# Kernel optimization log

Measured on AMD Instinct MI355X. Metric: run time of the kernel, lower is better.

## Reference

```python
import jax, jax.numpy as jnp
import numpy as np

CAP_FACTOR = 1.25


def _moe_top1(x, wg, w1, b1, w2, b2):
    """Top-1 switch MoE with capacity-based token dropping.
    x: [T, d]; wg: [d, E]; w1: [E, d, f]; b1: [E, f]; w2: [E, f, d]; b2: [E, d].
    """
    T, d = x.shape
    E = wg.shape[1]
    cap = int(CAP_FACTOR * T / E)
    probs = jax.nn.softmax(x @ wg, axis=-1)            # [T, E]
    idx = jnp.argmax(probs, axis=-1)                   # [T] expert assignment
    gate = jnp.max(probs, axis=-1)                     # [T] gate prob
    oh = jax.nn.one_hot(idx, E, dtype=jnp.int32)       # [T, E]
    # position of each token within its expert's buffer
    pos = (jnp.cumsum(oh, axis=0) * oh).sum(-1) - 1    # [T]
    keep = pos < cap                                   # drop tokens over capacity
    pos_w = jnp.where(keep, pos, cap)                  # dropped -> overflow slot
    # dispatch: scatter tokens into per-expert buffers [E, cap+1, d]
    buf = jnp.zeros((E, cap + 1, d), dtype=x.dtype).at[idx, pos_w].set(x)
    buf = buf[:, :cap]                                 # slice off overflow slot
    # grouped expert FFN
    h = jax.nn.relu(jnp.einsum('ecd,edf->ecf', buf, w1) + b1[:, None, :])
    eo = jnp.einsum('ecf,efd->ecd', h, w2) + b2[:, None, :]
    # combine: gather each token's expert output, scale by gate prob, zero dropped
    pos_g = jnp.minimum(pos_w, cap - 1)
    out = eo[idx, pos_g] * (gate * keep.astype(x.dtype))[:, None]
    return out


def setup_inputs():
    key = jax.random.key(0)
    ks = jax.random.split(key, 12)
    B, S, d, dff, E1, E2 = 8, 2048, 1024, 4096, 8, 16
    s = lambda fan: np.float32(1.0 / np.sqrt(fan))
    return dict(
        x=jax.random.normal(ks[0], (B, S, d), jnp.float32),
        y=jax.random.randint(ks[1], (B,), 0, d),
        wg1=jax.random.normal(ks[2], (d, E1), jnp.float32) * s(d),
        w1a=jax.random.normal(ks[3], (E1, d, dff), jnp.float32) * s(d),
        b1a=jnp.zeros((E1, dff), jnp.float32),
        w2a=jax.random.normal(ks[4], (E1, dff, d), jnp.float32) * s(dff),
        b2a=jnp.zeros((E1, d), jnp.float32),
        wg2=jax.random.normal(ks[5], (d, E2), jnp.float32) * s(d),
        w1b=jax.random.normal(ks[6], (E2, d, dff), jnp.float32) * s(d),
        b1b=jnp.zeros((E2, dff), jnp.float32),
        w2b=jax.random.normal(ks[7], (E2, dff, d), jnp.float32) * s(dff),
        b2b=jnp.zeros((E2, d), jnp.float32),
    )


def reference(x, y, wg1, w1a, b1a, w2a, b2a, wg2, w1b, b1b, w2b, b2b):
    B, S, d = x.shape
    xf = x.reshape(B * S, d)
    m1 = _moe_top1(xf, wg1, w1a, b1a, w2a, b2a)        # moe1(x)
    m2 = _moe_top1(m1, wg2, w1b, b1b, w2b, b2b)        # moe2(moe_out)
    resid = x + m2.reshape(B, S, d)                    # residual add
    sent = resid.mean(axis=1)                          # [B, d] mean-pool -> logits
    logp = jax.nn.log_softmax(sent, axis=-1)
    return -logp[jnp.arange(B), y].mean()              # cross-entropy loss
```

## Files before the change

### kernel.cpp

```cpp
#include <hip/hip_runtime.h>
#include <hip/hip_bf16.h>
#include <cstdint>
#include <cstddef>

#define B_    8
#define S_    2048
#define D_    1024
#define DFF_  4096
#define E1_   8
#define E2_   16
#define T_    (B_*S_)
#define CAP1_ 2560
#define CAP2_ 1280
#define EC_   20480

typedef __bf16 bf16x8 __attribute__((ext_vector_type(8)));
typedef float  f32x4  __attribute__((ext_vector_type(4)));

__device__ __forceinline__ unsigned short f2bf(float x) {
  return __builtin_bit_cast(unsigned short, (__bf16)x);
}

template<int E>
__global__ __launch_bounds__(256)
void gate_kernel(const float* __restrict__ X, const float* __restrict__ WG,
                 int* __restrict__ idxO, float* __restrict__ gateO) {
  const int lane = threadIdx.x & 63;
  const int wv   = threadIdx.x >> 6;
  const int t    = blockIdx.x * 4 + wv;
  const float* xr = X + (size_t)t * D_;
  float acc[E];
#pragma unroll
  for (int e = 0; e < E; ++e) acc[e] = 0.f;
#pragma unroll
  for (int i = 0; i < 4; ++i) {
    float4 xv = *(const float4*)(xr + i * 256 + lane * 4);
    int kb = i * 256 + lane * 4;
#pragma unroll
    for (int j = 0; j < 4; ++j) {
      float xs = (&xv.x)[j];
      const float* wr = WG + (size_t)(kb + j) * E;
#pragma unroll
      for (int e = 0; e < E; ++e) acc[e] += xs * wr[e];
    }
  }
#pragma unroll
  for (int e = 0; e < E; ++e) {
    float v = acc[e];
#pragma unroll
    for (int s = 32; s >= 1; s >>= 1) v += __shfl_xor(v, s, 64);
    acc[e] = v;
  }
  if (lane == 0) {
    float mx = acc[0]; int mi = 0;
#pragma unroll
    for (int e = 1; e < E; ++e) if (acc[e] > mx) { mx = acc[e]; mi = e; }
    float s = 0.f;
#pragma unroll
    for (int e = 0; e < E; ++e) s += expf(acc[e] - mx);
    idxO[t]  = mi;
    gateO[t] = 1.0f / s;
  }
}

__global__ __launch_bounds__(1024)
void scan_kernel(const int* __restrict__ idx, int E, int cap,
                 int* __restrict__ pos, int* __restrict__ kept) {
  __shared__ int cnt[16][17];
  __shared__ int gbase[16];
  const int tid = threadIdx.x;
  const int w = tid >> 6, lane = tid & 63;
  if (tid < E) gbase[tid] = 0;
  __syncthreads();
  const unsigned long long lt = (lane == 63) ? 0xFFFFFFFFFFFFFFFFull >> 1
                                             : ((1ull << lane) - 1ull);
  for (int it = 0; it < T_ / 1024; ++it) {
    int t = it * 1024 + tid;
    int mi = idx[t];
    int rank = 0;
    for (int e = 0; e < E; ++e) {
      unsigned long long m = __ballot(mi == e);
      if (lane == 0) cnt[w][e] = __popcll(m);
      if (mi == e) rank = __popcll(m & lt);
    }
    __syncthreads();
    int off = 0;
    for (int w2 = 0; w2 < w; ++w2) off += cnt[w2][mi];
    pos[t] = gbase[mi] + off + rank;
    __syncthreads();
    if (tid < E) {
      int tot = 0;
      for (int w2 = 0; w2 < 16; ++w2) tot += cnt[w2][tid];
      gbase[tid] += tot;
    }
    __syncthreads();
  }
  if (tid < E) kept[tid] = min(gbase[tid], cap);
}

__global__ __launch_bounds__(64)
void scatter_kernel(const float* __restrict__ X, const int* __restrict__ idx,
                    const int* __restrict__ pos, int cap,
                    unsigned short* __restrict__ xbuf, int* __restrict__ tokmap,
                    float* __restrict__ mzero) {
  const int t = blockIdx.x;
  const int lane = threadIdx.x;
  const int p = pos[t];
  if (p < cap) {
    const size_t dst = ((size_t)idx[t] * cap + p) * D_;
    const float* xr = X + (size_t)t * D_;
#pragma unroll
    for (int i = 0; i < 4; ++i) {
      float4 v = *(const float4*)(xr + i * 256 + lane * 4);
      ushort4 o;
      o.x = f2bf(v.x); o.y = f2bf(v.y); o.z = f2bf(v.z); o.w = f2bf(v.w);
      *(ushort4*)(xbuf + dst + i * 256 + lane * 4) = o;
    }
    if (lane == 0) tokmap[(size_t)idx[t] * cap + p] = t;
  } else {
    float4 z = {0.f, 0.f, 0.f, 0.f};
    float* mr = mzero + (size_t)t * D_;
#pragma unroll
    for (int i = 0; i < 4; ++i) *(float4*)(mr + i * 256 + lane * 4) = z;
  }
}

__global__ __launch_bounds__(256)
void wtrans_kernel(const float* __restrict__ src, unsigned short* __restrict__ dst,
                   int K, int N) {
  __shared__ float t[64][65];
  const int tid = threadIdx.x;
  const size_t eo = (size_t)blockIdx.z * K * N;
  const int k0 = blockIdx.y * 64, n0 = blockIdx.x * 64;
  const float* s = src + eo + (size_t)k0 * N + n0;
  unsigned short* d = dst + eo + (size_t)n0 * K + k0;
#pragma unroll
  for (int i = 0; i < 4; ++i) {
    int k = i * 16 + (tid >> 4);
    int n4 = (tid & 15) * 4;
    float4 v = *(const float4*)(s + (size_t)k * N + n4);
    t[k][n4] = v.x; t[k][n4 + 1] = v.y; t[k][n4 + 2] = v.z; t[k][n4 + 3] = v.w;
  }
  __syncthreads();
#pragma unroll
  for (int i = 0; i < 4; ++i) {
    int n = i * 16 + (tid >> 4);
    int k4 = (tid & 15) * 4;
    ushort4 o;
    o.x = f2bf(t[k4][n]);     o.y = f2bf(t[k4 + 1][n]);
    o.z = f2bf(t[k4 + 2][n]); o.w = f2bf(t[k4 + 3][n]);
    *(ushort4*)(d + (size_t)n * K + k4) = o;
  }
}

#define STG(BASEPTR, H, KT, SLOT) do {                                          \
    const unsigned short* _s = (BASEPTR) + (size_t)((H) * 128) * K + (KT) + st_off; \
    __builtin_amdgcn_global_load_lds((const __attribute__((address_space(1))) void*)_s, \
        (__attribute__((address_space(3))) void*)(smem + (SLOT) + dst0), 16, 0, 0);   \
    __builtin_amdgcn_global_load_lds((const __attribute__((address_space(1))) void*)(_s + (size_t)64 * K), \
        (__attribute__((address_space(3))) void*)(smem + (SLOT) + 8192 + dst0), 16, 0, 0); \
  } while (0)

#define RDA(BUF, MH) do { _Pragma("unroll")                                     \
    for (int m_ = 0; m_ < 4; ++m_) {                                            \
      const char* _p = smem + (BUF) * 65536 + aslot + ((MH) * 4 + m_) * 2048;   \
      af[m_][0] = *(const bf16x8*)(_p + va);                                    \
      af[m_][1] = *(const bf16x8*)(_p + (va ^ 64)); } } while (0)

#define RDB(BUF, NH) do { _Pragma("unroll")                                     \
    for (int j_ = 0; j_ < 2; ++j_) {                                            \
      const char* _p = smem + (BUF) * 65536 + bslot + ((NH) * 2 + j_) * 2048;   \
      bf[(NH) * 2 + j_][0] = *(const bf16x8*)(_p + vb);                         \
      bf[(NH) * 2 + j_][1] = *(const bf16x8*)(_p + (vb ^ 64)); } } while (0)

#define QUAD(MH, NH) do {                                                       \
    __builtin_amdgcn_s_setprio(1);                                              \
    _Pragma("unroll") for (int m_ = 0; m_ < 4; ++m_)                            \
    _Pragma("unroll") for (int j_ = 0; j_ < 2; ++j_)                            \
    _Pragma("unroll") for (int k_ = 0; k_ < 2; ++k_)                            \
      acc[(MH) * 4 + m_][(NH) * 2 + j_] = __builtin_amdgcn_mfma_f32_16x16x32_bf16( \
          af[m_][k_], bf[(NH) * 2 + j_][k_], acc[(MH) * 4 + m_][(NH) * 2 + j_], 0, 0, 0); \
    __builtin_amdgcn_s_setprio(0);                                              \
  } while (0)

#define LGKM0 do { asm volatile("s_waitcnt lgkmcnt(0)" ::: "memory");           \
                   __builtin_amdgcn_sched_barrier(0); } while (0)
#define BAR   __builtin_amdgcn_s_barrier()
#define VM4   asm volatile("s_waitcnt vmcnt(4)" ::: "memory")
#define VM0   asm volatile("s_waitcnt vmcnt(0)" ::: "memory")

template<int MODE>
__global__ __launch_bounds__(512, 2)
void moe_gemm(const unsigned short* __restrict__ A,
              const unsigned short* __restrict__ BT,
              const float* __restrict__ bias, int K, int N, int cap, int nbcnt,
              const int* __restrict__ kept,
              unsigned short* __restrict__ Hout, float* __restrict__ Mout,
              const int* __restrict__ tokmap, const float* __restrict__ gate) {
  __shared__ char smem[131072];
  const int tid  = threadIdx.x;
  const int lane = tid & 63;
  const int wv   = tid >> 6;
  const int wr   = wv >> 2;
  const int wc   = wv & 3;

  const int nwg = gridDim.x;
  const int wg  = (blockIdx.x & 7) * (nwg >> 3) + (blockIdx.x >> 3);
  const int per_grp = nbcnt * 4;
  const int grp = wg / per_grp;
  const int rem = wg - grp * per_grp;
  const int mb  = grp * 4 + (rem & 3);
  const int nb  = rem >> 2;

  const int e  = (mb * 256) / cap;
  const int r0 = mb * 256 - e * cap;
  const int kept_e = kept[e];
  if (r0 >= kept_e) return;
  const unsigned short* Ab = A + (size_t)(mb * 256) * K;
  const unsigned short* Bb = BT + ((size_t)e * N + (size_t)nb * 256) * K;

  f32x4 acc[8][4];
#pragma unroll
  for (int m = 0; m < 8; ++m)
#pragma unroll
    for (int n = 0; n < 4; ++n) acc[m][n] = (f32x4){0.f, 0.f, 0.f, 0.f};

  const int scol   = ((tid & 7) ^ ((tid >> 3) & 7)) * 8;
  const size_t st_off = (size_t)(tid >> 3) * K + scol;
  const int dst0   = tid * 16;

  const int r16 = lane & 15;
  const int g16 = (lane >> 4) * 16;
  const int swz = (r16 & 7) * 16;
  const int va  = r16 * 128 + (g16 ^ swz);
  const int vb  = (wc & 1) * 8192 + va;
  const int aslot = wr * 16384;
  const int bslot = 32768 + (wc >> 1) * 16384;
  bf16x8 af[4][2], bf[4][2];

  STG(Ab, 0, 0, 0);
  STG(Ab, 1, 0, 16384);
  STG(Bb, 0, 0, 32768);
  STG(Bb, 1, 0, 49152);
  STG(Bb, 0, 64, 65536 + 32768);
  STG(Bb, 1, 64, 65536 + 49152);
  VM4; BAR;

  const int NI = K >> 7;
  for (int i = 0; i < NI; ++i) {
    const bool last = (i == NI - 1);
    const int kt1 = (2 * i + 1) << 6;
    const int kt2 = (2 * i + 2) << 6;
    const int kt3 = (2 * i + 3) << 6;

    RDA(0, 0); RDB(0, 0);
    STG(Ab, 0, kt1, 65536);
    BAR; LGKM0; QUAD(0, 0); BAR;
    RDB(0, 1);
    STG(Ab, 1, kt1, 65536 + 16384);
    BAR; LGKM0; QUAD(0, 1); BAR;
    RDA(0, 1);
    if (!last) STG(Bb, 0, kt2, 32768);
    BAR; LGKM0; QUAD(1, 1); BAR;
    if (!last) { STG(Bb, 1, kt2, 49152); VM4; } else { VM0; }
    BAR; __builtin_amdgcn_sched_barrier(0);
    QUAD(1, 0); BAR;
    RDA(1, 0); RDB(1, 0);
    if (!last) STG(Ab, 0, kt2, 0);
    BAR; LGKM0; QUAD(0, 0); BAR;
    RDB(1, 1);
    if (!last) STG(Ab, 1, kt2, 16384);
    BAR; LGKM0; QUAD(0, 1); BAR;
    RDA(1, 1);
    if (!last) STG(Bb, 0, kt3, 65536 + 32768);
    BAR; LGKM0; QUAD(1, 1); BAR;
    if (!last) { STG(Bb, 1, kt3, 65536 + 49152); VM4; }
    BAR; __builtin_amdgcn_sched_barrier(0);
    QUAD(1, 0); BAR;
  }

  const int rg = lane >> 4;
  float bv[4];
#pragma unroll
  for (int n = 0; n < 4; ++n)
    bv[n] = bias[(size_t)e * N + nb * 256 + wc * 64 + n * 16 + r16];

#pragma unroll
  for (int m = 0; m < 8; ++m) {
#pragma unroll
    for (int r = 0; r < 4; ++r) {
      const int lrow = wr * 128 + m * 16 + rg * 4 + r;
      if (MODE == 0) {
        unsigned short* orow = Hout + (size_t)(mb * 256 + lrow) * N + nb * 256;
#pragma unroll
        for (int n = 0; n < 4; ++n) {
          float v = acc[m][n][r] + bv[n];
          orow[wc * 64 + n * 16 + r16] = f2bf(fmaxf(v, 0.f));
        }
      } else {
        const int lr = r0 + lrow;
        if (lr < kept_e) {
          const int tok = tokmap[mb * 256 + lrow];
          const float gsc = gate[tok];
          float* orow = Mout + (size_t)tok * N + nb * 256;
#pragma unroll
          for (int n = 0; n < 4; ++n)
            orow[wc * 64 + n * 16 + r16] = (acc[m][n][r] + bv[n]) * gsc;
        }
      }
    }
  }
}

__global__ __launch_bounds__(256)
void reduce_kernel(const float* __restrict__ X, const float* __restrict__ M2,
                   float* __restrict__ sent) {
  const int c = blockIdx.x * 256 + threadIdx.x;
  const int b = blockIdx.z;
  const int s0 = blockIdx.y * 128;
  float a = 0.f;
  size_t base = ((size_t)b * S_ + s0) * D_ + c;
  for (int s = 0; s < 128; ++s) a += X[base + (size_t)s * D_] + M2[base + (size_t)s * D_];
  atomicAdd(&sent[b * D_ + c], a * (1.0f / (float)S_));
}

__global__ __launch_bounds__(64)
void loss_kernel(const float* __restrict__ sent, const int* __restrict__ y,
                 float* __restrict__ out) {
  const int lane = threadIdx.x;
  float total = 0.f;
  for (int b = 0; b < B_; ++b) {
    const float* s = sent + b * D_;
    float v[16];
    float mx = -1e30f;
#pragma unroll
    for (int i = 0; i < 16; ++i) { v[i] = s[lane + i * 64]; mx = fmaxf(mx, v[i]); }
#pragma unroll
    for (int sh = 32; sh >= 1; sh >>= 1) mx = fmaxf(mx, __shfl_xor(mx, sh, 64));
    float sm = 0.f;
#pragma unroll
    for (int i = 0; i < 16; ++i) sm += expf(v[i] - mx);
#pragma unroll
    for (int sh = 32; sh >= 1; sh >>= 1) sm += __shfl_xor(sm, sh, 64);
    total += logf(sm) + mx - s[y[b]];
  }
  if (lane == 0) out[0] = total * (1.0f / (float)B_);
}

extern "C" void kernel_launch(void* const* d_in, const int* in_sizes, int n_in,
                              void* d_out, int out_size, void* d_ws, size_t ws_size,
                              hipStream_t stream) {
  const float* x   = (const float*)d_in[0];
  const int*   y   = (const int*)d_in[1];
  const float* wg1 = (const float*)d_in[2];
  const float* w1a = (const float*)d_in[3];
  const float* b1a = (const float*)d_in[4];
  const float* w2a = (const float*)d_in[5];
  const float* b2a = (const float*)d_in[6];
  const float* wg2 = (const float*)d_in[7];
  const float* w1b = (const float*)d_in[8];
  const float* b1b = (const float*)d_in[9];
  const float* w2b = (const float*)d_in[10];
  const float* b2b = (const float*)d_in[11];
  float* out = (float*)d_out;
  (void)in_sizes; (void)n_in; (void)out_size; (void)ws_size;

  char* base = (char*)d_ws;
  size_t o = 0;
  auto alloc = [&](size_t bytes) { size_t r = o; o = (o + bytes + 255) & ~(size_t)255; return r; };
  int*   idx1    = (int*)  (base + alloc((size_t)T_ * 4));
  int*   pos1    = (int*)  (base + alloc((size_t)T_ * 4));
  float* gate1   = (float*)(base + alloc((size_t)T_ * 4));
  int*   idx2    = (int*)  (base + alloc((size_t)T_ * 4));
  int*   pos2    = (int*)  (base + alloc((size_t)T_ * 4));
  float* gate2   = (float*)(base + alloc((size_t)T_ * 4));
  int*   kept1   = (int*)  (base + alloc(64 * 4));
  int*   kept2   = (int*)  (base + alloc(64 * 4));
  int*   tokmap1 = (int*)  (base + alloc((size_t)EC_ * 4));
  int*   tokmap2 = (int*)  (base + alloc((size_t)EC_ * 4));
  float* sent    = (float*)(base + alloc((size_t)B_ * D_ * 4));
  float* m1      = (float*)(base + alloc((size_t)T_ * D_ * 4));
  unsigned short* xbuf = (unsigned short*)(base + alloc((size_t)EC_ * D_ * 2));
  unsigned short* h    = (unsigned short*)(base + alloc((size_t)EC_ * DFF_ * 2));
  unsigned short* wT   = (unsigned short*)(base + alloc((size_t)E2_ * D_ * DFF_ * 2));

  hipMemsetAsync(sent, 0, (size_t)B_ * D_ * 4, stream);

  gate_kernel<E1_><<<T_ / 4, 256, 0, stream>>>(x, wg1, idx1, gate1);
  scan_kernel<<<1, 1024, 0, stream>>>(idx1, E1_, CAP1_, pos1, kept1);
  scatter_kernel<<<T_, 64, 0, stream>>>(x, idx1, pos1, CAP1_, xbuf, tokmap1, m1);
  wtrans_kernel<<<dim3(DFF_ / 64, D_ / 64, E1_), 256, 0, stream>>>(w1a, wT, D_, DFF_);
  moe_gemm<0><<<(DFF_ / 256) * (EC_ / 256), 512, 0, stream>>>(
      xbuf, wT, b1a, D_, DFF_, CAP1_, DFF_ / 256, kept1, h, nullptr, nullptr, nullptr);
  wtrans_kernel<<<dim3(D_ / 64, DFF_ / 64, E1_), 256, 0, stream>>>(w2a, wT, DFF_, D_);
  moe_gemm<1><<<(D_ / 256) * (EC_ / 256), 512, 0, stream>>>(
      h, wT, b2a, DFF_, D_, CAP1_, D_ / 256, kept1, nullptr, m1, tokmap1, gate1);

  gate_kernel<E2_><<<T_ / 4, 256, 0, stream>>>(m1, wg2, idx2, gate2);
  scan_kernel<<<1, 1024, 0, stream>>>(idx2, E2_, CAP2_, pos2, kept2);
  scatter_kernel<<<T_, 64, 0, stream>>>(m1, idx2, pos2, CAP2_, xbuf, tokmap2, m1);
  wtrans_kernel<<<dim3(DFF_ / 64, D_ / 64, E2_), 256, 0, stream>>>(w1b, wT, D_, DFF_);
  moe_gemm<0><<<(DFF_ / 256) * (EC_ / 256), 512, 0, stream>>>(
      xbuf, wT, b1b, D_, DFF_, CAP2_, DFF_ / 256, kept2, h, nullptr, nullptr, nullptr);
  wtrans_kernel<<<dim3(D_ / 64, DFF_ / 64, E2_), 256, 0, stream>>>(w2b, wT, DFF_, D_);
  moe_gemm<1><<<(D_ / 256) * (EC_ / 256), 512, 0, stream>>>(
      h, wT, b2b, DFF_, D_, CAP2_, D_ / 256, kept2, nullptr, m1, tokmap2, gate2);

  reduce_kernel<<<dim3(D_ / 256, S_ / 128, B_), 256, 0, stream>>>(x, m1, sent);
  loss_kernel<<<1, 64, 0, stream>>>(sent, y, out);
}
```

Baseline: 1.293 ms.

## Deepen global-to-LDS prefetch so A and B tiles load further ahead

```diff
diff --git a/kernel.cpp b/kernel.cpp
--- a/kernel.cpp
+++ b/kernel.cpp
@@ -185,8 +185,10 @@
 
 #define LGKM0 do { asm volatile("s_waitcnt lgkmcnt(0)" ::: "memory");           \
                    __builtin_amdgcn_sched_barrier(0); } while (0)
+#define LGKM8 asm volatile("s_waitcnt lgkmcnt(8)" ::: "memory")
 #define BAR   __builtin_amdgcn_s_barrier()
-#define VM4   asm volatile("s_waitcnt vmcnt(4)" ::: "memory")
+#define VM6   asm volatile("s_waitcnt vmcnt(6)" ::: "memory")
+#define VM8   asm volatile("s_waitcnt vmcnt(8)" ::: "memory")
 #define VM0   asm volatile("s_waitcnt vmcnt(0)" ::: "memory")
 
 template<int MODE>
@@ -238,43 +240,51 @@
   const int bslot = 32768 + (wc >> 1) * 16384;
   bf16x8 af[4][2], bf[4][2];
 
+
   STG(Ab, 0, 0, 0);
-  STG(Ab, 1, 0, 16384);
   STG(Bb, 0, 0, 32768);
   STG(Bb, 1, 0, 49152);
-  STG(Bb, 0, 64, 65536 + 32768);
-  STG(Bb, 1, 64, 65536 + 49152);
-  VM4; BAR;
-
+  STG(Ab, 1, 0, 16384);
+  STG(Ab, 0, 64, 65536);
+  STG(Bb, 0, 64, 98304);
+  STG(Bb, 1, 64, 114688);
+  STG(Ab, 1, 64, 81920);
+  VM8; BAR;
+
+  const int NT = K >> 6;
   const int NI = K >> 7;
   for (int i = 0; i < NI; ++i) {
     const bool last = (i == NI - 1);
+    const bool s2 = (2 * i + 2) < NT;
+    const bool s3 = (2 * i + 3) < NT;
     const int kt1 = (2 * i + 1) << 6;
     const int kt2 = (2 * i + 2) << 6;
     const int kt3 = (2 * i + 3) << 6;
 
     RDA(0, 0); RDB(0, 0);
-    STG(Ab, 0, kt1, 65536);
-    BAR; LGKM0; QUAD(0, 0); BAR;
+    if (i > 0) STG(Ab, 1, kt1, 81920);
+    LGKM8; BAR; LGKM0; QUAD(0, 0); BAR;
     RDB(0, 1);
-    STG(Ab, 1, kt1, 65536 + 16384);
+    if (s2) STG(Ab, 0, kt2, 0);
     BAR; LGKM0; QUAD(0, 1); BAR;
     RDA(0, 1);
-    if (!last) STG(Bb, 0, kt2, 32768);
+    if (s2) STG(Bb, 0, kt2, 32768);
     BAR; LGKM0; QUAD(1, 1); BAR;
-    if (!last) { STG(Bb, 1, kt2, 49152); VM4; } else { VM0; }
+    if (s2) STG(Bb, 1, kt2, 49152);
+    if (last) { VM0; } else { VM6; }
     BAR; __builtin_amdgcn_sched_barrier(0);
     QUAD(1, 0); BAR;
     RDA(1, 0); RDB(1, 0);
-    if (!last) STG(Ab, 0, kt2, 0);
-    BAR; LGKM0; QUAD(0, 0); BAR;
+    if (s2) STG(Ab, 1, kt2, 16384);
+    LGKM8; BAR; LGKM0; QUAD(0, 0); BAR;
     RDB(1, 1);
-    if (!last) STG(Ab, 1, kt2, 16384);
+    if (s3) STG(Ab, 0, kt3, 65536);
     BAR; LGKM0; QUAD(0, 1); BAR;
     RDA(1, 1);
-    if (!last) STG(Bb, 0, kt3, 65536 + 32768);
+    if (s3) STG(Bb, 0, kt3, 98304);
     BAR; LGKM0; QUAD(1, 1); BAR;
-    if (!last) { STG(Bb, 1, kt3, 65536 + 49152); VM4; }
+    if (s3) STG(Bb, 1, kt3, 114688);
+    if (!last) VM6;
     BAR; __builtin_amdgcn_sched_barrier(0);
     QUAD(1, 0); BAR;
   }
```

Result: no change. 1.298 ms (+0.4%).
